# Performance work log

Measured on AMD Instinct MI355X. Metric: run time of the kernel, lower is better.

The kernel has to match this reference:

```python
import jax, jax.numpy as jnp
import numpy as np

N_NODES = 50000
IN_CH = 128
OUT_CH = 64
N_EDGES = 800000


def setup_inputs() -> dict:
    key = jax.random.key(0)
    k1, k2, k3, k4 = jax.random.split(key, 4)
    z = jax.random.normal(k1, (N_NODES, IN_CH), dtype=jnp.float32)
    edge_index = jax.random.randint(k2, (2, N_EDGES), 0, N_NODES, dtype=jnp.int64)
    # GCNConv params: weight [in, out] (glorot-ish), bias [out]
    W = jax.random.normal(k3, (IN_CH, OUT_CH), dtype=jnp.float32) / np.sqrt(IN_CH)
    b = jnp.zeros((OUT_CH,), dtype=jnp.float32)
    return {"z": z, "edge_index": edge_index, "W": W, "b": b}


def reference(z, edge_index, W, b):
    N = z.shape[0]
    # linear transform first (out_channels < in_channels reduces message traffic)
    x = z @ W  # [N, out]
    # add self-loops
    loop = jnp.arange(N, dtype=edge_index.dtype)
    src = jnp.concatenate([edge_index[0], loop])
    dst = jnp.concatenate([edge_index[1], loop])
    # symmetric normalization deg^-1/2 (degree counted on dst, incl. self-loops)
    deg = jnp.zeros((N,), dtype=x.dtype).at[dst].add(1.0)
    dinv = jnp.where(deg > 0, jax.lax.rsqrt(deg), 0.0)
    norm = dinv[src] * dinv[dst]  # [E+N]
    msg = x[src] * norm[:, None]  # gather + scale
    out = jax.ops.segment_sum(msg, dst, num_segments=N)  # scatter-add
    return jax.nn.relu(out + b)
```

## Files before the change

### kernel.cpp

```cpp
#include <hip/hip_runtime.h>
#include <hip/hip_bf16.h>

#define IN_CH 128
#define OUT_CH 64

#define CSHIFT 6
#define BNODES 64
#define NCMAX 1024
#define CAP 1536
#define BIN_EPT 8

typedef __attribute__((ext_vector_type(8))) short bf16x8;
typedef __attribute__((ext_vector_type(4))) float f32x4;

__device__ inline short f2bfs(float x) {
    __hip_bfloat16 h = __float2bfloat16(x);
    return __builtin_bit_cast(short, h);
}
__device__ inline float bf2f(unsigned short h) {
    unsigned int u = ((unsigned int)h) << 16;
    return __builtin_bit_cast(float, u);
}

__global__ void bin_edges(const int* __restrict__ ei, int* __restrict__ gctr,
                          unsigned int* __restrict__ ebuf, int E, int NC, int nbin,
                          const float* __restrict__ W, unsigned short* __restrict__ wf) {
    if (blockIdx.x == (unsigned)nbin) {
        for (int i = threadIdx.x; i < 4 * 4 * 64 * 8; i += blockDim.x) {
            int j    = i & 7;
            int lane = (i >> 3) & 63;
            int kk   = (i >> 9) & 3;
            int nt   = i >> 11;
            int k = kk * 32 + ((lane >> 4) & 3) * 8 + j;
            int n = nt * 16 + (lane & 15);
            wf[i] = (unsigned short)f2bfs(W[k * OUT_CH + n]);
        }
        return;
    }
    __shared__ int cnt[NCMAX];
    __shared__ int gbase[NCMAX];
    for (int i = threadIdx.x; i < NC; i += blockDim.x) cnt[i] = 0;
    __syncthreads();

    unsigned int pk[BIN_EPT];
    int bk[BIN_EPT];
    const int g0 = (blockIdx.x * blockDim.x + threadIdx.x) * BIN_EPT;

    if (g0 + BIN_EPT <= E) {
        int4 s0 = *(const int4*)(ei + g0);
        int4 s1 = *(const int4*)(ei + g0 + 4);
        int4 d0 = *(const int4*)(ei + E + g0);
        int4 d1 = *(const int4*)(ei + E + g0 + 4);
        int ss[BIN_EPT] = {s0.x, s0.y, s0.z, s0.w, s1.x, s1.y, s1.z, s1.w};
        int dd[BIN_EPT] = {d0.x, d0.y, d0.z, d0.w, d1.x, d1.y, d1.z, d1.w};
#pragma unroll
        for (int k = 0; k < BIN_EPT; ++k) {
            pk[k] = ((unsigned int)dd[k] << 16) | (unsigned int)ss[k];
            bk[k] = dd[k] >> CSHIFT;
            atomicAdd(&cnt[bk[k]], 1);
        }
    } else {
#pragma unroll
        for (int k = 0; k < BIN_EPT; ++k) {
            int e = g0 + k;
            if (e < E) {
                int s = ei[e];
                int d = ei[E + e];
                pk[k] = ((unsigned int)d << 16) | (unsigned int)s;
                bk[k] = d >> CSHIFT;
                atomicAdd(&cnt[bk[k]], 1);
            } else bk[k] = -1;
        }
    }
    __syncthreads();
    for (int i = threadIdx.x; i < NC; i += blockDim.x) {
        int c = cnt[i];
        gbase[i] = c ? atomicAdd(&gctr[i], c) : 0;
    }
    __syncthreads();
    for (int i = threadIdx.x; i < NC; i += blockDim.x) cnt[i] = 0;
    __syncthreads();
#pragma unroll
    for (int k = 0; k < BIN_EPT; ++k) {
        if (bk[k] >= 0) {
            int o = gbase[bk[k]] + atomicAdd(&cnt[bk[k]], 1);
            if (o < CAP)
                ebuf[(size_t)bk[k] * CAP + o] = pk[k];
        }
    }
}

__global__ __launch_bounds__(256) void sort_gemm(const unsigned int* __restrict__ ebuf,
                                                 const int* __restrict__ gctr,
                                                 const float* __restrict__ z,
                                                 const unsigned short* __restrict__ wfrag,
                                                 int* __restrict__ boff,
                                                 unsigned short* __restrict__ gscol,
                                                 unsigned short* __restrict__ y, int N) {
    __shared__ unsigned int epk[CAP];
    __shared__ unsigned short scolL[CAP];
    __shared__ int cnt[BNODES];
    __shared__ int off[BNODES];
    __shared__ float dinvL[BNODES];
    const int b = blockIdx.x;
    const int tid = threadIdx.x;
    const int n0 = b << CSHIFT;
    const int ecnt = min(gctr[b], CAP);
    const unsigned int* eb = ebuf + (size_t)b * CAP;

    if (tid < BNODES) cnt[tid] = 0;
    __syncthreads();
    for (int i = tid; i < ecnt; i += 256) {
        unsigned int p = eb[i];
        epk[i] = p;
        atomicAdd(&cnt[(int)(p >> 16) - n0], 1);
    }
    __syncthreads();

    int deg = 0;
    if (tid < BNODES) { deg = cnt[tid]; off[tid] = deg; }
    __syncthreads();
    for (int o = 1; o < BNODES; o <<= 1) {
        int v = (tid < BNODES && tid >= o) ? off[tid - o] : 0;
        __syncthreads();
        if (tid < BNODES) off[tid] += v;
        __syncthreads();
    }
    if (tid < BNODES) {
        int ex = off[tid] - deg;
        boff[b * BNODES + tid] = ex;
        cnt[tid] = ex;
        dinvL[tid] = rsqrtf((float)(deg + 1));
    }
    __syncthreads();

    for (int i = tid; i < ecnt; i += 256) {
        unsigned int p = epk[i];
        int rel = (int)(p >> 16) - n0;
        int slot = atomicAdd(&cnt[rel], 1);
        scolL[slot] = (unsigned short)(p & 0xFFFFu);
    }
    __syncthreads();
    for (int i = tid; i < ecnt; i += 256)
        gscol[(size_t)b * CAP + i] = scolL[i];

    const int lane = tid & 63;
    const int wid  = tid >> 6;
    const int row0 = n0 + wid * 16;

    bf16x8 bfr[4][4];
#pragma unroll
    for (int nt = 0; nt < 4; ++nt)
#pragma unroll
        for (int kk = 0; kk < 4; ++kk)
            bfr[nt][kk] = *(const bf16x8*)&wfrag[(((nt * 4 + kk) * 64) + lane) * 8];

    f32x4 acc[4];
#pragma unroll
    for (int nt = 0; nt < 4; ++nt) acc[nt] = (f32x4){0.f, 0.f, 0.f, 0.f};

    const int arow = row0 + (lane & 15);
    const int zrow = (arow < N) ? arow : (N - 1);
    const int sub  = lane >> 4;
    const float* zr = z + (size_t)zrow * IN_CH + sub * 8;

#pragma unroll
    for (int kk = 0; kk < 4; ++kk) {
        float4 f0 = *(const float4*)(zr + kk * 32);
        float4 f1 = *(const float4*)(zr + kk * 32 + 4);
        bf16x8 a;
        a[0] = f2bfs(f0.x); a[1] = f2bfs(f0.y);
        a[2] = f2bfs(f0.z); a[3] = f2bfs(f0.w);
        a[4] = f2bfs(f1.x); a[5] = f2bfs(f1.y);
        a[6] = f2bfs(f1.z); a[7] = f2bfs(f1.w);
#pragma unroll
        for (int nt = 0; nt < 4; ++nt)
            acc[nt] = __builtin_amdgcn_mfma_f32_16x16x32_bf16(a, bfr[nt][kk], acc[nt], 0, 0, 0);
    }

    const int rrel0 = wid * 16 + sub * 4;
#pragma unroll
    for (int r = 0; r < 4; ++r) {
        int row = n0 + rrel0 + r;
        if (row < N) {
            float di = dinvL[rrel0 + r];
#pragma unroll
            for (int nt = 0; nt < 4; ++nt)
                y[(size_t)row * OUT_CH + nt * 16 + (lane & 15)] =
                    (unsigned short)f2bfs(acc[nt][r] * di);
        }
    }
}

__global__ __launch_bounds__(512) void gather(const int* __restrict__ gctr,
                                              const int* __restrict__ boff,
                                              const unsigned short* __restrict__ gscol,
                                              const unsigned int* __restrict__ y2,
                                              const float* __restrict__ bias,
                                              float* __restrict__ out, int N) {
    __shared__ unsigned short scol[CAP];
    __shared__ int off_s[BNODES + 1];
    const int b = blockIdx.x;
    const int n0 = b << CSHIFT;
    const int tid = threadIdx.x;
    const int ecnt = min(gctr[b], CAP);

    if (tid < BNODES) off_s[tid] = boff[b * BNODES + tid];
    if (tid == 0) off_s[BNODES] = ecnt;
    __syncthreads();
    {
        const unsigned int* gs32 = (const unsigned int*)(gscol + (size_t)b * CAP);
        unsigned int* sc32 = (unsigned int*)scol;
        for (int i = tid; i < (ecnt + 1) / 2; i += 512) sc32[i] = gs32[i];
    }
    __syncthreads();

    const int lane = tid & 63;
    const int w = tid >> 6;
    const int half = lane >> 5;
    const int c2 = lane & 31;
    const float2 bv = *(const float2*)&bias[c2 * 2];

#pragma unroll
    for (int rnd = 0; rnd < 4; ++rnd) {
        const int nrel = rnd * 16 + w * 2 + half;
        const int node = n0 + nrel;
        const bool valid = node < N;
        int jbeg = valid ? off_s[nrel] : 0;
        int cend = valid ? off_s[nrel + 1] : 0;
        const float di = rsqrtf((float)(cend - jbeg + 1));

        float accLo = 0.f, accHi = 0.f;
        if (valid) {
            unsigned int sv = y2[(size_t)node * 32 + c2];
            accLo = bf2f((unsigned short)(sv & 0xFFFFu));
            accHi = bf2f((unsigned short)(sv >> 16));
        }

        for (int j = jbeg; j < cend; j += 8) {
            unsigned int v[8]; bool m[8];
#pragma unroll
            for (int t = 0; t < 8; ++t) {
                int jj = j + t;
                m[t] = jj < cend;
                int s = scol[m[t] ? jj : (cend - 1)];
                v[t] = y2[(size_t)s * 32 + c2];
            }
#pragma unroll
            for (int t = 0; t < 8; ++t) {
                if (m[t]) {
                    accLo += bf2f((unsigned short)(v[t] & 0xFFFFu));
                    accHi += bf2f((unsigned short)(v[t] >> 16));
                }
            }
        }

        if (valid) {
            float2 o2;
            o2.x = fmaxf(fmaf(accLo, di, bv.x), 0.f);
            o2.y = fmaxf(fmaf(accHi, di, bv.y), 0.f);
            *(float2*)&out[(size_t)node * OUT_CH + c2 * 2] = o2;
        }
    }
}

extern "C" void kernel_launch(void* const* d_in, const int* in_sizes, int n_in,
                              void* d_out, int out_size, void* d_ws, size_t ws_size,
                              hipStream_t stream) {
    const float* z  = (const float*)d_in[0];
    const int*   ei = (const int*)d_in[1];
    const float* W  = (const float*)d_in[2];
    const float* b  = (const float*)d_in[3];
    float*       out = (float*)d_out;

    const int N = in_sizes[0] / IN_CH;
    const int E = in_sizes[1] / 2;
    const int NC = (N + BNODES - 1) >> CSHIFT;

    unsigned short* y     = (unsigned short*)d_ws;
    unsigned int*   ebuf  = (unsigned int*)(y + (size_t)N * OUT_CH);
    unsigned short* gscol = (unsigned short*)(ebuf + (size_t)NC * CAP);
    int*            boff  = (int*)(gscol + (size_t)NC * CAP);
    int*            gctr  = boff + (size_t)NC * BNODES;
    unsigned short* wfrag = (unsigned short*)(((uintptr_t)(gctr + NC) + 15) & ~(uintptr_t)15);

    hipMemsetAsync(gctr, 0, (size_t)NC * sizeof(int), stream);

    const int binBlocks = (E + 256 * BIN_EPT - 1) / (256 * BIN_EPT);

    bin_edges<<<binBlocks + 1, 256, 0, stream>>>(ei, gctr, ebuf, E, NC, binBlocks, W, wfrag);
    sort_gemm<<<NC, 256, 0, stream>>>(ebuf, gctr, z, wfrag, boff, gscol, y, N);
    gather   <<<NC, 512, 0, stream>>>(gctr, boff, gscol, (const unsigned int*)y, b, out, N);
}
```

Before: 66.36 us.

## Fuse sort/GEMM and gather into one cooperative kernel with grid sync

Merges the per-bucket edge sort plus bf16 MFMA transform with the neighbor gather into a single cooperative kernel, separated by a grid-wide sync. Sorted column indices and CSR offsets stay in LDS instead of being written to and re-read from global memory, and one launch boundary is removed. In exchange, the gather phase runs with 256 threads per block instead of 512 and pays for a grid barrier. The fused path is taken only if an occupancy check, which assumes 256 CUs, shows the whole grid can be resident; otherwise the old two-kernel path runs.

```diff
diff --git a/kernel.cpp b/kernel.cpp
--- a/kernel.cpp
+++ b/kernel.cpp
@@ -1,5 +1,8 @@
 #include <hip/hip_runtime.h>
 #include <hip/hip_bf16.h>
+#include <hip/hip_cooperative_groups.h>
+
+namespace cg = cooperative_groups;
 
 #define IN_CH 128
 #define OUT_CH 64
@@ -86,6 +89,157 @@
             int o = gbase[bk[k]] + atomicAdd(&cnt[bk[k]], 1);
             if (o < CAP)
                 ebuf[(size_t)bk[k] * CAP + o] = pk[k];
+        }
+    }
+}
+
+__global__ __launch_bounds__(256) void fused_sg(const unsigned int* __restrict__ ebuf,
+                                                const int* __restrict__ gctr,
+                                                const float* __restrict__ z,
+                                                const unsigned short* __restrict__ wfrag,
+                                                unsigned short* __restrict__ y,
+                                                const float* __restrict__ bias,
+                                                float* __restrict__ out, int N) {
+    __shared__ unsigned int epk[CAP];
+    __shared__ unsigned short scolL[CAP];
+    __shared__ int cnt[BNODES];
+    __shared__ int offE[BNODES + 1];
+    __shared__ float dinvL[BNODES];
+    const int b = blockIdx.x;
+    const int tid = threadIdx.x;
+    const int n0 = b << CSHIFT;
+    const int ecnt = min(gctr[b], CAP);
+    const unsigned int* eb = ebuf + (size_t)b * CAP;
+
+    if (tid < BNODES) cnt[tid] = 0;
+    __syncthreads();
+    for (int i = tid; i < ecnt; i += 256) {
+        unsigned int p = eb[i];
+        epk[i] = p;
+        atomicAdd(&cnt[(int)(p >> 16) - n0], 1);
+    }
+    __syncthreads();
+
+    int deg = 0;
+    if (tid < BNODES) {
+        deg = cnt[tid];
+        offE[tid + 1] = deg;
+        if (tid == 0) offE[0] = 0;
+    }
+    __syncthreads();
+    for (int o = 1; o < BNODES; o <<= 1) {
+        int v = (tid < BNODES && tid >= o) ? offE[tid + 1 - o] : 0;
+        __syncthreads();
+        if (tid < BNODES) offE[tid + 1] += v;
+        __syncthreads();
+    }
+    if (tid < BNODES) {
+        cnt[tid] = offE[tid];
+        dinvL[tid] = rsqrtf((float)(deg + 1));
+    }
+    __syncthreads();
+
+    for (int i = tid; i < ecnt; i += 256) {
+        unsigned int p = epk[i];
+        int rel = (int)(p >> 16) - n0;
+        int slot = atomicAdd(&cnt[rel], 1);
+        scolL[slot] = (unsigned short)(p & 0xFFFFu);
+    }
+
+    const int lane = tid & 63;
+    const int wid  = tid >> 6;
+    const int row0 = n0 + wid * 16;
+
+    bf16x8 bfr[4][4];
+#pragma unroll
+    for (int nt = 0; nt < 4; ++nt)
+#pragma unroll
+        for (int kk = 0; kk < 4; ++kk)
+            bfr[nt][kk] = *(const bf16x8*)&wfrag[(((nt * 4 + kk) * 64) + lane) * 8];
+
+    f32x4 acc[4];
+#pragma unroll
+    for (int nt = 0; nt < 4; ++nt) acc[nt] = (f32x4){0.f, 0.f, 0.f, 0.f};
+
+    const int arow = row0 + (lane & 15);
+    const int zrow = (arow < N) ? arow : (N - 1);
+    const int sub  = lane >> 4;
+    const float* zr = z + (size_t)zrow * IN_CH + sub * 8;
+
+#pragma unroll
+    for (int kk = 0; kk < 4; ++kk) {
+        float4 f0 = *(const float4*)(zr + kk * 32);
+        float4 f1 = *(const float4*)(zr + kk * 32 + 4);
+        bf16x8 a;
+        a[0] = f2bfs(f0.x); a[1] = f2bfs(f0.y);
+        a[2] = f2bfs(f0.z); a[3] = f2bfs(f0.w);
+        a[4] = f2bfs(f1.x); a[5] = f2bfs(f1.y);
+        a[6] = f2bfs(f1.z); a[7] = f2bfs(f1.w);
+#pragma unroll
+        for (int nt = 0; nt < 4; ++nt)
+            acc[nt] = __builtin_amdgcn_mfma_f32_16x16x32_bf16(a, bfr[nt][kk], acc[nt], 0, 0, 0);
+    }
+
+    __syncthreads();
+    const int rrel0 = wid * 16 + sub * 4;
+#pragma unroll
+    for (int r = 0; r < 4; ++r) {
+        int row = n0 + rrel0 + r;
+        if (row < N) {
+            float di = dinvL[rrel0 + r];
+#pragma unroll
+            for (int nt = 0; nt < 4; ++nt)
+                y[(size_t)row * OUT_CH + nt * 16 + (lane & 15)] =
+                    (unsigned short)f2bfs(acc[nt][r] * di);
+        }
+    }
+
+    cg::this_grid().sync();
+
+    const int half = lane >> 5;
+    const int c2 = lane & 31;
+    const float2 bv = *(const float2*)&bias[c2 * 2];
+    const unsigned int* y2 = (const unsigned int*)y;
+
+#pragma unroll
+    for (int rnd = 0; rnd < 8; ++rnd) {
+        const int nrel = rnd * 8 + wid * 2 + half;
+        const int node = n0 + nrel;
+        const bool valid = node < N;
+        const int jbeg = valid ? offE[nrel] : 0;
+        const int cend = valid ? offE[nrel + 1] : 0;
+        const float di = dinvL[nrel];
+
+        float accLo = 0.f, accHi = 0.f;
+        if (valid) {
+            unsigned int sv = y2[(size_t)node * 32 + c2];
+            accLo = bf2f((unsigned short)(sv & 0xFFFFu));
+            accHi = bf2f((unsigned short)(sv >> 16));
+        }
+
+        for (int j = jbeg; j < cend; j += 8) {
+            unsigned int v[8]; bool m[8];
+#pragma unroll
+            for (int t = 0; t < 8; ++t) {
+                int jj = j + t;
+                m[t] = jj < cend;
+                int s = scolL[m[t] ? jj : (cend - 1)];
+                v[t] = y2[(size_t)s * 32 + c2];
+            }
+#pragma unroll
+            for (int t = 0; t < 8; ++t) {
+                if (m[t]) {
+                    accLo += bf2f((unsigned short)(v[t] & 0xFFFFu));
+                    accHi += bf2f((unsigned short)(v[t] >> 16));
+                }
+            }
+        }
+
+        if (valid) {
+            float2 o2;
+            o2.x = fmaxf(fmaf(accLo, di, bv.x), 0.f);
+            o2.y = fmaxf(fmaf(accHi, di, bv.y), 0.f);
+            *(float2*)&out[(size_t)node * OUT_CH + c2 * 2] = o2;
         }
     }
 }
@@ -289,6 +443,25 @@
     const int binBlocks = (E + 256 * BIN_EPT - 1) / (256 * BIN_EPT);
 
     bin_edges<<<binBlocks + 1, 256, 0, stream>>>(ei, gctr, ebuf, E, NC, binBlocks, W, wfrag);
+
+    int blocksPerCU = 0;
+    hipError_t qerr = hipOccupancyMaxActiveBlocksPerMultiprocessor(
+        &blocksPerCU, (const void*)fused_sg, 256, 0);
+    bool coop_ok = (qerr == hipSuccess) && (blocksPerCU * 256  >= NC);
+
+    if (coop_ok) {
+        const unsigned int* ebuf_c = ebuf;
+        const int* gctr_c = gctr;
+        const unsigned short* wfrag_c = wfrag;
+        const float* bias_c = b;
+        int N_c = N;
+        void* kargs[] = {(void*)&ebuf_c, (void*)&gctr_c, (void*)&z, (void*)&wfrag_c,
+                         (void*)&y, (void*)&bias_c, (void*)&out, (void*)&N_c};
+        hipError_t lerr = hipLaunchCooperativeKernel((const void*)fused_sg,
+                                                     dim3(NC), dim3(256), kargs, 0, stream);
+        if (lerr == hipSuccess) return;
+    }
+
     sort_gemm<<<NC, 256, 0, stream>>>(ebuf, gctr, z, wfrag, boff, gscol, y, N);
     gather   <<<NC, 512, 0, stream>>>(gctr, boff, gscol, (const unsigned int*)y, b, out, N);
 }
```

Measured after the change: 66.38 us. About the same (+0.0%).
